# Performance work log

Hardware: AMD Instinct MI355X
Metric: run time of the kernel (lower is better)

The kernel has to match this reference:

```python
import jax, jax.numpy as jnp
import numpy as np

N, E, IN_FT, OUT_FT = 20000, 4096, 128, 128


def setup_inputs() -> dict:
    key = jax.random.key(0)
    kx, kh, kw = jax.random.split(key, 3)
    X = jax.random.normal(kx, (N, IN_FT), dtype=jnp.float32)
    H = jax.random.randint(kh, (N, E), 0, 2, dtype=jnp.int32)
    weight = jax.random.normal(kw, (IN_FT, OUT_FT), dtype=jnp.float32) * (1.0 / np.sqrt(IN_FT))
    bias = jnp.zeros((OUT_FT,), dtype=jnp.float32)
    return {"X": X, "H": H, "weight": weight, "bias": bias}


def reference(X, H, weight, bias):
    # Dv^{-1/2} H De^{-1} H^T Dv^{-1/2} X W + b, with diag matrices fused as
    # row/column scalings (same math as the torch.diag @ chain, no NxN temporaries).
    Hf = H.astype(jnp.float32)
    v_deg = jnp.sum(Hf, axis=1)            # [N]
    e_deg = jnp.sum(Hf, axis=0)            # [E]
    v_deg = jnp.where(v_deg > 0, v_deg, 1.0)
    e_deg = jnp.where(e_deg > 0, e_deg, 1.0)
    dv_inv_sqrt = 1.0 / jnp.sqrt(v_deg)    # diag(Dv^-1/2)
    de_inv = 1.0 / e_deg                   # diag(De^-1)
    Y = dv_inv_sqrt[:, None] * X
    T = Hf.T @ Y                           # H^T (...)        [E, in]
    T = de_inv[:, None] * T                # De^-1 (...)
    Z = Hf @ T                             # H (...)          [N, in]
    Z = dv_inv_sqrt[:, None] * Z           # Dv^-1/2 (...)
    out = Z @ weight + bias                # [N, out]
    return out
```

## Files before the change

kernel.cpp:

```cpp
#include <hip/hip_runtime.h>

#define NV 20000
#define NE 4096
#define FT 128
#define NW_E 128
#define NW_V 625
#define NVP 20032

typedef __attribute__((ext_vector_type(8))) short short8v;
typedef __attribute__((ext_vector_type(4))) float float4v;

__device__ __forceinline__ unsigned short f2bf(float f) {
    unsigned u = __float_as_uint(f);
    u += 0x7FFFu + ((u >> 16) & 1u);
    return (unsigned short)(u >> 16);
}
__device__ __forceinline__ int lds_off(int r, int chunk) {
    return r * 128 + ((chunk ^ (r & 7)) << 4);
}
__device__ __forceinline__ uint4 lut_entry(int t) {
    uint4 e;
    e.x = ((t & 1) ? 0x3F80u : 0u) | ((t & 2) ? 0x3F800000u : 0u);
    e.y = ((t & 4) ? 0x3F80u : 0u) | ((t & 8) ? 0x3F800000u : 0u);
    e.z = ((t & 16) ? 0x3F80u : 0u) | ((t & 32) ? 0x3F800000u : 0u);
    e.w = ((t & 64) ? 0x3F80u : 0u) | ((t & 128) ? 0x3F800000u : 0u);
    return e;
}

__global__ __launch_bounds__(256) void k_packt(const int* __restrict__ H,
                                               unsigned* __restrict__ packed,
                                               unsigned* __restrict__ packedT,
                                               int* __restrict__ dvp) {
    __shared__ int cl[64];
    int b = blockIdx.x;
    int g = b >> 1, h = b & 1;
    int t = threadIdx.x, lane = t & 63;
    int w0 = h * 64 + (t >> 6) * 16;
    int n = g * 64 + lane;
    bool valid = n < NV;
    const uint4* base = reinterpret_cast<const uint4*>(H) + (size_t)n * (NE / 4);

    if (t < 64) cl[t] = 0;
    __syncthreads();

    int cnt = 0;
    int nw = g * 2 + (lane >> 5);
    for (int it = 0; it < 16; ++it) {
        int w = w0 + it;
        unsigned m = 0;
        if (valid) {
            const uint4* p = base + w * 8;
#pragma unroll
            for (int i = 0; i < 8; ++i) {
                uint4 v = p[i];
                m |= (v.x ? 1u : 0u) << (i * 4 + 0);
                m |= (v.y ? 1u : 0u) << (i * 4 + 1);
                m |= (v.z ? 1u : 0u) << (i * 4 + 2);
                m |= (v.w ? 1u : 0u) << (i * 4 + 3);
            }
            packed[(size_t)n * NW_E + w] = m;
        }
        cnt += __popc(m);
        unsigned my = 0;
#pragma unroll
        for (int j = 0; j < 32; ++j) {
            unsigned long long bm = __ballot(((m >> j) & 1u) != 0);
            unsigned part = (lane < 32) ? (unsigned)bm : (unsigned)(bm >> 32);
            if ((lane & 31) == j) my = part;
        }
        int e = w * 32 + (lane & 31);
        if (nw < NW_V) packedT[(size_t)e * NW_V + nw] = my;
    }
    atomicAdd(&cl[lane], cnt);
    __syncthreads();
    if (t < 64) dvp[h * NVP + g * 64 + t] = cl[t];
}

__global__ __launch_bounds__(64) void k_deg(const unsigned* __restrict__ packedT,
                                            const int* __restrict__ dvp,
                                            float* __restrict__ de,
                                            float* __restrict__ dv) {
    int bid = blockIdx.x, l = threadIdx.x;
    if (bid < NE) {
        const unsigned* row = packedT + (size_t)bid * NW_V;
        int c = 0;
        for (int i = l; i < NW_V; i += 64) c += __popc(row[i]);
        for (int o = 32; o > 0; o >>= 1) c += __shfl_down(c, o, 64);
        if (l == 0) de[bid] = c > 0 ? 1.0f / (float)c : 1.0f;
    } else {
        int i = (bid - NE) * 64 + l;
        if (i < NV) {
            int d = dvp[i] + dvp[NVP + i];
            dv[i] = d > 0 ? 1.0f / sqrtf((float)d) : 1.0f;
        }
    }
}

__global__ __launch_bounds__(256) void k_ybft(const float* __restrict__ X,
                                              const float* __restrict__ dv,
                                              unsigned short* __restrict__ Ybf) {
    int t = threadIdx.x;
    int f = t & 127;
    int nb = (blockIdx.x * 2 + (t >> 7)) * 8;
    unsigned short h[8];
#pragma unroll
    for (int i = 0; i < 8; ++i) {
        float v = X[(size_t)(nb + i) * FT + f] * dv[nb + i];
        h[i] = f2bf(v);
    }
    uint4 u;
    u.x = (unsigned)h[0] | ((unsigned)h[1] << 16);
    u.y = (unsigned)h[2] | ((unsigned)h[3] << 16);
    u.z = (unsigned)h[4] | ((unsigned)h[5] << 16);
    u.w = (unsigned)h[6] | ((unsigned)h[7] << 16);
    *reinterpret_cast<uint4*>(Ybf + (size_t)f * NV + nb) = u;
}

__global__ __launch_bounds__(256, 2) void k_mm1(const unsigned short* __restrict__ Ybf,
                                                const unsigned* __restrict__ packedT,
                                                float* __restrict__ P, int chunkK) {
    __shared__ __align__(16) unsigned char sA[128 * 128];
    __shared__ __align__(16) unsigned char sB[128 * 128];
    __shared__ __align__(16) uint4 slut[256];
    int t = threadIdx.x;
    slut[t] = lut_entry(t & 255);
    if (t < 256 - 256) {}

    int et = blockIdx.x & 31, kp = blockIdx.x >> 5;
    int e0 = et * 128;
    int kbeg = kp * chunkK;
    int iters = chunkK >> 6;

    float4v acc[4][4];
#pragma unroll
    for (int i = 0; i < 4; ++i)
#pragma unroll
        for (int j = 0; j < 4; ++j)
#pragma unroll
            for (int r = 0; r < 4; ++r) acc[i][j][r] = 0.0f;

    int fA = t & 127;
    int chbA = (t >> 7) * 4;
    const unsigned short* arow = Ybf + (size_t)fA * NV;
    int eB = t & 127;
    int hB = t >> 7;
    const unsigned* brow = packedT + (size_t)(e0 + eB) * NW_V;

    int wave = t >> 6, lane = t & 63;
    int wm0 = (wave & 1) * 64, wc0 = (wave >> 1) * 64;
    int r0 = lane & 15, q = lane >> 4;
    __syncthreads();

    for (int it = 0; it < iters; ++it) {
        int k0 = kbeg + it * 64;
#pragma unroll
        for (int c = 0; c < 4; ++c) {
            int ch = chbA + c;
            int n = k0 + ch * 8;
            uint4 v = {0, 0, 0, 0};
            if (n < NV) v = *reinterpret_cast<const uint4*>(arow + n);
            *reinterpret_cast<uint4*>(sA + lds_off(fA, ch)) = v;
        }
        {
            int nw = (k0 >> 5) + hB;
            unsigned wv = (nw < NW_V) ? brow[nw] : 0u;
#pragma unroll
            for (int c = 0; c < 4; ++c) {
                uint4 u = slut[(wv >> (c * 8)) & 0xFF];
                *reinterpret_cast<uint4*>(sB + lds_off(eB, hB * 4 + c)) = u;
            }
        }
        __syncthreads();
#pragma unroll
        for (int ks = 0; ks < 2; ++ks) {
            short8v a[4], bb[4];
#pragma unroll
            for (int mi = 0; mi < 4; ++mi)
                a[mi] = *reinterpret_cast<const short8v*>(sA + lds_off(wm0 + mi * 16 + r0, ks * 4 + q));
#pragma unroll
            for (int ci = 0; ci < 4; ++ci)
                bb[ci] = *reinterpret_cast<const short8v*>(sB + lds_off(wc0 + ci * 16 + r0, ks * 4 + q));
#pragma unroll
            for (int mi = 0; mi < 4; ++mi)
#pragma unroll
                for (int ci = 0; ci < 4; ++ci)
                    acc[mi][ci] = __builtin_amdgcn_mfma_f32_16x16x32_bf16(a[mi], bb[ci], acc[mi][ci], 0, 0, 0);
        }
        __syncthreads();
    }
    float* Pp = P + (size_t)kp * (128 * 4096);
#pragma unroll
    for (int mi = 0; mi < 4; ++mi)
#pragma unroll
        for (int ci = 0; ci < 4; ++ci) {
            int f = wm0 + mi * 16 + q * 4;
            int e = e0 + wc0 + ci * 16 + r0;
#pragma unroll
            for (int r = 0; r < 4; ++r)
                Pp[(size_t)(f + r) * 4096 + e] = acc[mi][ci][r];
        }
}

__global__ __launch_bounds__(256) void k_reduce(const float4v* __restrict__ P,
                                                float4v* __restrict__ Tt, int S) {
    int i = blockIdx.x * 256 + threadIdx.x;
    float4v a = P[i];
    for (int p = 1; p < S; ++p) a += P[(size_t)p * 131072 + i];
    Tt[i] = a;
}

__global__ __launch_bounds__(256) void k_ut(const float* __restrict__ Tt,
                                            const float* __restrict__ W,
                                            const float* __restrict__ de,
                                            unsigned short* __restrict__ Ubf) {
    int t = threadIdx.x;
    int e = blockIdx.x * 64 + (t & 63);
    int g0 = blockIdx.y * 16 + (t >> 6) * 4;
    float a0 = 0, a1 = 0, a2 = 0, a3 = 0;
    for (int f = 0; f < 128; ++f) {
        float tv = Tt[(size_t)f * 4096 + e];
        float4 wv = *reinterpret_cast<const float4*>(W + f * 128 + g0);
        a0 += tv * wv.x; a1 += tv * wv.y; a2 += tv * wv.z; a3 += tv * wv.w;
    }
    float d = de[e];
    Ubf[(size_t)(g0 + 0) * 4096 + e] = f2bf(a0 * d);
    Ubf[(size_t)(g0 + 1) * 4096 + e] = f2bf(a1 * d);
    Ubf[(size_t)(g0 + 2) * 4096 + e] = f2bf(a2 * d);
    Ubf[(size_t)(g0 + 3) * 4096 + e] = f2bf(a3 * d);
}

__global__ __launch_bounds__(256, 2) void k_mm2(const unsigned* __restrict__ packed,
                                                const unsigned short* __restrict__ Ubf,
                                                const float* __restrict__ dv,
                                                const float* __restrict__ bias,
                                                float* __restrict__ out) {
    __shared__ __align__(16) unsigned char sA[128 * 128];
    __shared__ __align__(16) unsigned char sB[64 * 128];
    __shared__ __align__(16) uint4 slut[256];
    int t = threadIdx.x;
    slut[t] = lut_entry(t & 255);

    int mt = blockIdx.x >> 1, half = blockIdx.x & 1;
    int n0 = mt * 128, g0 = half * 64;

    float4v acc[4][2];
#pragma unroll
    for (int i = 0; i < 4; ++i)
#pragma unroll
        for (int j = 0; j < 2; ++j)
#pragma unroll
            for (int r = 0; r < 4; ++r) acc[i][j][r] = 0.0f;

    int nA = t & 127, hA = t >> 7;
    int gB = t & 63, chbB = (t >> 6) * 2;
    const unsigned short* brow = Ubf + (size_t)(g0 + gB) * 4096;

    int wave = t >> 6, lane = t & 63;
    int wm0 = (wave & 1) * 64, wc0 = (wave >> 1) * 32;
    int r0 = lane & 15, q = lane >> 4;
    __syncthreads();

    for (int k0 = 0; k0 < 4096; k0 += 64) {
        {
            unsigned wv = (n0 + nA < NV) ? packed[(size_t)(n0 + nA) * NW_E + (k0 >> 5) + hA] : 0u;
#pragma unroll
            for (int c = 0; c < 4; ++c) {
                uint4 u = slut[(wv >> (c * 8)) & 0xFF];
                *reinterpret_cast<uint4*>(sA + lds_off(nA, hA * 4 + c)) = u;
            }
        }
#pragma unroll
        for (int c = 0; c < 2; ++c) {
            int ch = chbB + c;
            uint4 v = *reinterpret_cast<const uint4*>(brow + k0 + ch * 8);
            *reinterpret_cast<uint4*>(sB + lds_off(gB, ch)) = v;
        }
        __syncthreads();
#pragma unroll
        for (int ks = 0; ks < 2; ++ks) {
            short8v a[4], bb[2];
#pragma unroll
            for (int mi = 0; mi < 4; ++mi)
                a[mi] = *reinterpret_cast<const short8v*>(sA + lds_off(wm0 + mi * 16 + r0, ks * 4 + q));
#pragma unroll
            for (int ci = 0; ci < 2; ++ci)
                bb[ci] = *reinterpret_cast<const short8v*>(sB + lds_off(wc0 + ci * 16 + r0, ks * 4 + q));
#pragma unroll
            for (int mi = 0; mi < 4; ++mi)
#pragma unroll
                for (int ci = 0; ci < 2; ++ci)
                    acc[mi][ci] = __builtin_amdgcn_mfma_f32_16x16x32_bf16(a[mi], bb[ci], acc[mi][ci], 0, 0, 0);
        }
        __syncthreads();
    }
#pragma unroll
    for (int ci = 0; ci < 2; ++ci) {
        int g = g0 + wc0 + ci * 16 + r0;
        float bg = bias[g];
#pragma unroll
        for (int mi = 0; mi < 4; ++mi) {
#pragma unroll
            for (int r = 0; r < 4; ++r) {
                int n = n0 + wm0 + mi * 16 + q * 4 + r;
                if (n < NV) out[(size_t)n * 128 + g] = dv[n] * acc[mi][ci][r] + bg;
            }
        }
    }
}

extern "C" void kernel_launch(void* const* d_in, const int* in_sizes, int n_in,
                              void* d_out, int out_size, void* d_ws, size_t ws_size,
                              hipStream_t stream) {
    const float* X    = (const float*)d_in[0];
    const int*   H    = (const int*)d_in[1];
    const float* W    = (const float*)d_in[2];
    const float* bias = (const float*)d_in[3];
    float* out = (float*)d_out;

    char* ws = (char*)d_ws;
    size_t off = 0;
    auto alloc = [&](size_t sz) { char* p = ws + off; off += (sz + 255) & ~(size_t)255; return p; };
    unsigned*       packed  = (unsigned*)alloc((size_t)NV * NW_E * 4);
    unsigned*       packedT = (unsigned*)alloc((size_t)NE * NW_V * 4);
    unsigned short* Ybf     = (unsigned short*)alloc((size_t)FT * NV * 2);
    float*          Tt      = (float*)alloc((size_t)FT * NE * 4);
    unsigned short* Ubf     = (unsigned short*)alloc((size_t)FT * NE * 2);
    float*          dv      = (float*)alloc((size_t)NV * 4);
    float*          de      = (float*)alloc((size_t)NE * 4);
    int*            dvp     = (int*)alloc((size_t)2 * NVP * 4);
    size_t fixed = off;

    long long avail = (long long)ws_size - (long long)fixed;
    int S = (int)(avail / (128LL * 4096 * 4));
    if (S > 16) S = 16;
    if (S < 1) S = 1;
    float* P1 = (float*)(ws + fixed);
    int chunkK = ((NV + S * 64 - 1) / (S * 64)) * 64;

    k_packt <<<626, 256, 0, stream>>>(H, packed, packedT, dvp);
    k_deg   <<<NE + 313, 64, 0, stream>>>(packedT, dvp, de, dv);
    k_ybft  <<<1250, 256, 0, stream>>>(X, dv, Ybf);
    k_mm1   <<<32 * S, 256, 0, stream>>>(Ybf, packedT, P1, chunkK);
    k_reduce<<<512, 256, 0, stream>>>((const float4v*)P1, (float4v*)Tt, S);
    k_ut    <<<dim3(64, 8), 256, 0, stream>>>(Tt, W, de, Ubf);
    k_mm2   <<<314, 256, 0, stream>>>(packed, Ubf, dv, bias, out);
}
```

Baseline: 628.6 us.

## Fuse degree and Y-transpose kernels; split mm2 into quarter-column tiles

Merges k_deg and k_ybft into a single k_mid launch. The Y conversion blocks recompute the vertex degree scale directly from dvp, so they no longer depend on dv having been written earlier. Edge-degree work now packs four edges per 256-thread block. k_mm2 tiles 32 output columns instead of 64, doubling the grid to 628 blocks and allowing 4 blocks per CU, to raise occupancy on a grid that was small relative to the CU count. The cost is that each A tile (the H bit-expansion) is rebuilt twice as often, and there is less MFMA reuse per A load.

```diff
diff --git a/kernel.cpp b/kernel.cpp
--- a/kernel.cpp
+++ b/kernel.cpp
@@ -76,44 +76,46 @@
     if (t < 64) dvp[h * NVP + g * 64 + t] = cl[t];
 }
 
-__global__ __launch_bounds__(64) void k_deg(const unsigned* __restrict__ packedT,
-                                            const int* __restrict__ dvp,
-                                            float* __restrict__ de,
-                                            float* __restrict__ dv) {
-    int bid = blockIdx.x, l = threadIdx.x;
-    if (bid < NE) {
-        const unsigned* row = packedT + (size_t)bid * NW_V;
+__global__ __launch_bounds__(256) void k_mid(const unsigned* __restrict__ packedT,
+                                             const int* __restrict__ dvp,
+                                             const float* __restrict__ X,
+                                             float* __restrict__ de,
+                                             float* __restrict__ dv,
+                                             unsigned short* __restrict__ Ybf) {
+    int b = blockIdx.x, t = threadIdx.x;
+    if (b < 1024) {
+        int lane = t & 63, w = t >> 6;
+        int e = b * 4 + w;
+        const unsigned* row = packedT + (size_t)e * NW_V;
         int c = 0;
-        for (int i = l; i < NW_V; i += 64) c += __popc(row[i]);
+        for (int i = lane; i < NW_V; i += 64) c += __popc(row[i]);
         for (int o = 32; o > 0; o >>= 1) c += __shfl_down(c, o, 64);
-        if (l == 0) de[bid] = c > 0 ? 1.0f / (float)c : 1.0f;
-    } else {
-        int i = (bid - NE) * 64 + l;
+        if (lane == 0) de[e] = c > 0 ? 1.0f / (float)c : 1.0f;
+    } else if (b < 1024 + 79) {
+        int i = (b - 1024) * 256 + t;
         if (i < NV) {
             int d = dvp[i] + dvp[NVP + i];
             dv[i] = d > 0 ? 1.0f / sqrtf((float)d) : 1.0f;
         }
-    }
-}
-
-__global__ __launch_bounds__(256) void k_ybft(const float* __restrict__ X,
-                                              const float* __restrict__ dv,
-                                              unsigned short* __restrict__ Ybf) {
-    int t = threadIdx.x;
-    int f = t & 127;
-    int nb = (blockIdx.x * 2 + (t >> 7)) * 8;
-    unsigned short h[8];
-#pragma unroll
-    for (int i = 0; i < 8; ++i) {
-        float v = X[(size_t)(nb + i) * FT + f] * dv[nb + i];
-        h[i] = f2bf(v);
-    }
-    uint4 u;
-    u.x = (unsigned)h[0] | ((unsigned)h[1] << 16);
-    u.y = (unsigned)h[2] | ((unsigned)h[3] << 16);
-    u.z = (unsigned)h[4] | ((unsigned)h[5] << 16);
-    u.w = (unsigned)h[6] | ((unsigned)h[7] << 16);
-    *reinterpret_cast<uint4*>(Ybf + (size_t)f * NV + nb) = u;
+    } else {
+        int b2 = b - 1103;
+        int f = t & 127;
+        int nb = (b2 * 2 + (t >> 7)) * 8;
+        unsigned short h[8];
+#pragma unroll
+        for (int i = 0; i < 8; ++i) {
+            int n = nb + i;
+            int d = dvp[n] + dvp[NVP + n];
+            float s = d > 0 ? 1.0f / sqrtf((float)d) : 1.0f;
+            h[i] = f2bf(X[(size_t)n * FT + f] * s);
+        }
+        uint4 u;
+        u.x = (unsigned)h[0] | ((unsigned)h[1] << 16);
+        u.y = (unsigned)h[2] | ((unsigned)h[3] << 16);
+        u.z = (unsigned)h[4] | ((unsigned)h[5] << 16);
+        u.w = (unsigned)h[6] | ((unsigned)h[7] << 16);
+        *reinterpret_cast<uint4*>(Ybf + (size_t)f * NV + nb) = u;
+    }
 }
 
 __global__ __launch_bounds__(256, 2) void k_mm1(const unsigned short* __restrict__ Ybf,
@@ -124,7 +126,6 @@
     __shared__ __align__(16) uint4 slut[256];
     int t = threadIdx.x;
     slut[t] = lut_entry(t & 255);
-    if (t < 256 - 256) {}
 
     int et = blockIdx.x & 31, kp = blockIdx.x >> 5;
     int e0 = et * 128;
@@ -229,34 +230,32 @@
     Ubf[(size_t)(g0 + 3) * 4096 + e] = f2bf(a3 * d);
 }
 
-__global__ __launch_bounds__(256, 2) void k_mm2(const unsigned* __restrict__ packed,
+__global__ __launch_bounds__(256, 4) void k_mm2(const unsigned* __restrict__ packed,
                                                 const unsigned short* __restrict__ Ubf,
                                                 const float* __restrict__ dv,
                                                 const float* __restrict__ bias,
                                                 float* __restrict__ out) {
     __shared__ __align__(16) unsigned char sA[128 * 128];
-    __shared__ __align__(16) unsigned char sB[64 * 128];
+    __shared__ __align__(16) unsigned char sB[32 * 128];
     __shared__ __align__(16) uint4 slut[256];
     int t = threadIdx.x;
     slut[t] = lut_entry(t & 255);
 
-    int mt = blockIdx.x >> 1, half = blockIdx.x & 1;
-    int n0 = mt * 128, g0 = half * 64;
-
-    float4v acc[4][2];
+    int mt = blockIdx.x >> 2, qg = blockIdx.x & 3;
+    int n0 = mt * 128, g0 = qg * 32;
+
+    float4v acc[4];
 #pragma unroll
     for (int i = 0; i < 4; ++i)
 #pragma unroll
-        for (int j = 0; j < 2; ++j)
-#pragma unroll
-            for (int r = 0; r < 4; ++r) acc[i][j][r] = 0.0f;
+        for (int r = 0; r < 4; ++r) acc[i][r] = 0.0f;
 
     int nA = t & 127, hA = t >> 7;
-    int gB = t & 63, chbB = (t >> 6) * 2;
-    const unsigned short* brow = Ubf + (size_t)(g0 + gB) * 4096;
+    int rB = t & 31, cB = t >> 5;
+    const unsigned short* brow = Ubf + (size_t)(g0 + rB) * 4096;
 
     int wave = t >> 6, lane = t & 63;
-    int wm0 = (wave & 1) * 64, wc0 = (wave >> 1) * 32;
+    int wm0 = (wave & 1) * 64, wc0 = (wave >> 1) * 16;
     int r0 = lane & 15, q = lane >> 4;
     __syncthreads();
 
@@ -269,40 +268,33 @@
                 *reinterpret_cast<uint4*>(sA + lds_off(nA, hA * 4 + c)) = u;
             }
         }
-#pragma unroll
-        for (int c = 0; c < 2; ++c) {
-            int ch = chbB + c;
-            uint4 v = *reinterpret_cast<const uint4*>(brow + k0 + ch * 8);
-            *reinterpret_cast<uint4*>(sB + lds_off(gB, ch)) = v;
+        {
+            uint4 v = *reinterpret_cast<const uint4*>(brow + k0 + cB * 8);
+            *reinterpret_cast<uint4*>(sB + lds_off(rB, cB)) = v;
         }
         __syncthreads();
 #pragma unroll
         for (int ks = 0; ks < 2; ++ks) {
-            short8v a[4], bb[2];
+            short8v a[4], bb;
 #pragma unroll
             for (int mi = 0; mi < 4; ++mi)
                 a[mi] = *reinterpret_cast<const short8v*>(sA + lds_off(wm0 + mi * 16 + r0, ks * 4 + q));
-#pragma unroll
-            for (int ci = 0; ci < 2; ++ci)
-                bb[ci] = *reinterpret_cast<const short8v*>(sB + lds_off(wc0 + ci * 16 + r0, ks * 4 + q));
+            bb = *reinterpret_cast<const short8v*>(sB + lds_off(wc0 + r0, ks * 4 + q));
 #pragma unroll
             for (int mi = 0; mi < 4; ++mi)
-#pragma unroll
-                for (int ci = 0; ci < 2; ++ci)
-                    acc[mi][ci] = __builtin_amdgcn_mfma_f32_16x16x32_bf16(a[mi], bb[ci], acc[mi][ci], 0, 0, 0);
+                acc[mi] = __builtin_amdgcn_mfma_f32_16x16x32_bf16(a[mi], bb, acc[mi], 0, 0, 0);
         }
         __syncthreads();
     }
-#pragma unroll
-    for (int ci = 0; ci < 2; ++ci) {
-        int g = g0 + wc0 + ci * 16 + r0;
+    {
+        int g = g0 + wc0 + r0;
         float bg = bias[g];
 #pragma unroll
         for (int mi = 0; mi < 4; ++mi) {
 #pragma unroll
             for (int r = 0; r < 4; ++r) {
                 int n = n0 + wm0 + mi * 16 + q * 4 + r;
-                if (n < NV) out[(size_t)n * 128 + g] = dv[n] * acc[mi][ci][r] + bg;
+                if (n < NV) out[(size_t)n * 128 + g] = dv[n] * acc[mi][r] + bg;
             }
         }
     }
@@ -338,10 +330,9 @@
     int chunkK = ((NV + S * 64 - 1) / (S * 64)) * 64;
 
     k_packt <<<626, 256, 0, stream>>>(H, packed, packedT, dvp);
-    k_deg   <<<NE + 313, 64, 0, stream>>>(packedT, dvp, de, dv);
-    k_ybft  <<<1250, 256, 0, stream>>>(X, dv, Ybf);
+    k_mid   <<<2353, 256, 0, stream>>>(packedT, dvp, X, de, dv, Ybf);
     k_mm1   <<<32 * S, 256, 0, stream>>>(Ybf, packedT, P1, chunkK);
     k_reduce<<<512, 256, 0, stream>>>((const float4v*)P1, (float4v*)Tt, S);
     k_ut    <<<dim3(64, 8), 256, 0, stream>>>(Tt, W, de, Ubf);
-    k_mm2   <<<314, 256, 0, stream>>>(packed, Ubf, dv, bias, out);
-}
+    k_mm2   <<<628, 256, 0, stream>>>(packed, Ubf, dv, bias, out);
+}
```

After: 636.1 us. No clear change (+1.2%).
